# Kernel optimization log

Hardware: AMD Instinct MI355X
Metric: run time of the kernel (lower is better)

The kernel has to match this reference:

```python
import jax, jax.numpy as jnp
import numpy as np

N_OFFSETS = [(1, 0), (1, 1), (0, 1), (-1, 1), (-1, 0), (-1, -1), (0, -1), (1, -1)]
DILATION = 1


def setup_inputs() -> dict:
    key = jax.random.key(0)
    feats = jax.random.normal(key, (8, 128, 256, 256), dtype=jnp.float32)
    return {"feats": feats}


def reference(feats):
    # feats: [B, C, H, W]
    d = DILATION
    B, C, H, W = feats.shape
    # channel-wise L2 normalize (no eps, matching torch .norm division)
    normed = feats / jnp.linalg.norm(feats, axis=1, keepdims=True)
    # reflect pad last two spatial dims by d
    padded = jnp.pad(normed, ((0, 0), (0, 0), (d, d), (d, d)), mode="reflect")
    # 8 shifted multiply + channel-sum correlations (fixed small offset set)
    corrs = jnp.concatenate(
        [
            jnp.sum(
                normed
                * padded[:, :, d - dx * d // d if False else d - dx:H + d - dx, d - dy:W + d - dy],
                axis=1,
                keepdims=True,
            )
            for dx, dy in [(ox * d, oy * d) for ox, oy in N_OFFSETS]
        ],
        axis=1,
    )  # [B, 8, H, W]
    return corrs
```

## Files before the change

kernel.cpp:

```cpp
#include <hip/hip_runtime.h>


#define BB 8
#define CC 128
#define HH 256
#define WW 256
#define CSPLIT 2
#define CPW (CC / CSPLIT)

#define DD(k, j) acc[12 + (k)*4 + (j)]

__global__ __launch_bounds__(128) void featcorr_kernel(
    const float* __restrict__ feats, float* __restrict__ out) {
  const int lane = threadIdx.x;
  const int wy = threadIdx.y;
  const int h = (blockIdx.x % 8) * (HH / 8) + (blockIdx.x / 8);
  const int b = blockIdx.y;

  const int hm = (h == 0) ? 1 : h - 1;
  const int hp = (h == HH - 1) ? HH - 2 : h + 1;

  const size_t HW = (size_t)HH * WW;
  const int col0 = lane * 4;

  const float* pT = feats + ((size_t)b * CC + wy * CPW) * HW + (size_t)hm * WW + col0;
  const float* pM = feats + ((size_t)b * CC + wy * CPW) * HW + (size_t)h * WW + col0;
  const float* pB = feats + ((size_t)b * CC + wy * CPW) * HW + (size_t)hp * WW + col0;

  float acc[44];
#pragma unroll
  for (int a = 0; a < 44; ++a) acc[a] = 0.f;

  auto compute = [&](const float4 t, const float4 m, const float4 bt) {
    const float rT = __shfl_down(t.x, 1);
    const float rM = __shfl_down(m.x, 1);
    const float rB = __shfl_down(bt.x, 1);
    acc[0] += t.x * t.x;  acc[1] += t.y * t.y;  acc[2] += t.z * t.z;  acc[3] += t.w * t.w;
    acc[4] += m.x * m.x;  acc[5] += m.y * m.y;  acc[6] += m.z * m.z;  acc[7] += m.w * m.w;
    acc[8] += bt.x * bt.x; acc[9] += bt.y * bt.y; acc[10] += bt.z * bt.z; acc[11] += bt.w * bt.w;
    DD(0, 0) += m.x * t.x; DD(0, 1) += m.y * t.y; DD(0, 2) += m.z * t.z; DD(0, 3) += m.w * t.w;
    DD(4, 0) += m.x * bt.x; DD(4, 1) += m.y * bt.y; DD(4, 2) += m.z * bt.z; DD(4, 3) += m.w * bt.w;
    DD(1, 1) += m.y * t.x; DD(1, 2) += m.z * t.y; DD(1, 3) += m.w * t.z;
    DD(1, 0) += rM * t.w;
    DD(2, 1) += m.y * m.x; DD(2, 2) += m.z * m.y; DD(2, 3) += m.w * m.z;
    DD(2, 0) += rM * m.w;
    DD(3, 1) += m.y * bt.x; DD(3, 2) += m.z * bt.y; DD(3, 3) += m.w * bt.z;
    DD(3, 0) += rM * bt.w;
    DD(5, 0) += m.x * bt.y; DD(5, 1) += m.y * bt.z; DD(5, 2) += m.z * bt.w; DD(5, 3) += m.w * rB;
    DD(6, 0) += m.x * m.y; DD(6, 1) += m.y * m.z; DD(6, 2) += m.z * m.w; DD(6, 3) += m.w * rM;
    DD(7, 0) += m.x * t.y; DD(7, 1) += m.y * t.z; DD(7, 2) += m.z * t.w; DD(7, 3) += m.w * rT;
  };

  float4 tA = *(const float4*)pT, mA = *(const float4*)pM, bA = *(const float4*)pB;
  pT += HW; pM += HW; pB += HW;
  float4 tB = *(const float4*)pT, mB = *(const float4*)pM, bB = *(const float4*)pB;
  pT += HW; pM += HW; pB += HW;

#pragma unroll 2
  for (int c = 0; c < CPW - 2; ++c) {
    const float4 tC = *(const float4*)pT;
    const float4 mC = *(const float4*)pM;
    const float4 bC = *(const float4*)pB;
    pT += HW; pM += HW; pB += HW;
    compute(tA, mA, bA);
    tA = tB; mA = mB; bA = bB;
    tB = tC; mB = mC; bB = bC;
  }
  compute(tA, mA, bA);
  compute(tB, mB, bB);

  __shared__ float lds[44][64];
  if (wy == 1) {
#pragma unroll
    for (int a = 0; a < 44; ++a) lds[a][lane] = acc[a];
  }
  __syncthreads();

  if (wy == 0) {
#pragma unroll
    for (int a = 0; a < 44; ++a) acc[a] += lds[a][lane];

    const float g1 = __shfl_up(DD(1, 0), 1);
    const float g2 = __shfl_up(DD(2, 0), 1);
    const float g3 = __shfl_up(DD(3, 0), 1);
    DD(1, 0) = (lane == 0) ? DD(7, 0) : g1;
    DD(2, 0) = (lane == 0) ? DD(6, 0) : g2;
    DD(3, 0) = (lane == 0) ? DD(5, 0) : g3;
    if (lane == 63) {
      DD(5, 3) = DD(3, 3);
      DD(6, 3) = DD(2, 3);
      DD(7, 3) = DD(1, 3);
    }

    float it[4], im[4], ib[4];
#pragma unroll
    for (int j = 0; j < 4; ++j) {
      it[j] = rsqrtf(acc[j]);
      im[j] = rsqrtf(acc[4 + j]);
      ib[j] = rsqrtf(acc[8 + j]);
    }
    float IT[6], IM[6], IB[6];
    IT[1] = it[0]; IT[2] = it[1]; IT[3] = it[2]; IT[4] = it[3];
    IM[1] = im[0]; IM[2] = im[1]; IM[3] = im[2]; IM[4] = im[3];
    IB[1] = ib[0]; IB[2] = ib[1]; IB[3] = ib[2]; IB[4] = ib[3];
    const float tl = __shfl_up(it[3], 1), ml = __shfl_up(im[3], 1), bl = __shfl_up(ib[3], 1);
    const float tr = __shfl_down(it[0], 1), mr = __shfl_down(im[0], 1), br = __shfl_down(ib[0], 1);
    IT[0] = (lane == 0) ? it[1] : tl;
    IM[0] = (lane == 0) ? im[1] : ml;
    IB[0] = (lane == 0) ? ib[1] : bl;
    IT[5] = (lane == 63) ? it[2] : tr;
    IM[5] = (lane == 63) ? im[2] : mr;
    IB[5] = (lane == 63) ? ib[2] : br;

    float* obase = out + ((size_t)b * 8) * HW + (size_t)h * WW + col0;
#pragma unroll
    for (int k = 0; k < 8; ++k) {
      float v[4];
#pragma unroll
      for (int j = 0; j < 4; ++j) {
        float in;
        switch (k) {
          case 0: in = it[j];     break;
          case 1: in = IT[j];     break;
          case 2: in = IM[j];     break;
          case 3: in = IB[j];     break;
          case 4: in = ib[j];     break;
          case 5: in = IB[j + 2]; break;
          case 6: in = IM[j + 2]; break;
          default: in = IT[j + 2]; break;
        }
        v[j] = DD(k, j) * im[j] * in;
      }
      float4 o;
      o.x = v[0]; o.y = v[1]; o.z = v[2]; o.w = v[3];
      *(float4*)(obase + (size_t)k * HW) = o;
    }
  }
}

extern "C" void kernel_launch(void* const* d_in, const int* in_sizes, int n_in,
                              void* d_out, int out_size, void* d_ws, size_t ws_size,
                              hipStream_t stream) {
  const float* feats = (const float*)d_in[0];
  float* out = (float*)d_out;
  dim3 block(64, CSPLIT, 1);
  dim3 grid(HH, BB, 1);
  featcorr_kernel<<<grid, block, 0, stream>>>(feats, out);
}
```

Baseline: 365.8 us.

## Process four rows per block with LDS-staged shared halo rows

Each block now handles four output rows with eight wavefronts (four rows times two channel halves). Each wave loads one or two input rows per channel and stages them in double-buffered LDS so the six rows are shared, rather than every row reloading its three neighbours from global memory. The redundant DD(2,0) accumulation is dropped and recovered from DD(6,3) of the left lane. This cuts global read amplification from 3x to 1.5x, at the cost of two block barriers per channel pair and more LDS traffic.

Result: no change. 367.2 us (+0.4%).

```diff
diff --git a/kernel.cpp b/kernel.cpp
--- a/kernel.cpp
+++ b/kernel.cpp
@@ -5,33 +5,59 @@
 #define CC 128
 #define HH 256
 #define WW 256
-#define CSPLIT 2
-#define CPW (CC / CSPLIT)
+#define RR 4
+#define NV 6
+#define CPH (CC / 2)
 
 #define DD(k, j) acc[12 + (k)*4 + (j)]
 
-__global__ __launch_bounds__(128) void featcorr_kernel(
+union SmemU {
+  float stage[2][2][NV][WW];
+  float red[RR][44][64];
+};
+
+__global__ __launch_bounds__(512) void featcorr_kernel(
     const float* __restrict__ feats, float* __restrict__ out) {
+  __shared__ SmemU sm;
   const int lane = threadIdx.x;
   const int wy = threadIdx.y;
-  const int h = (blockIdx.x % 8) * (HH / 8) + (blockIdx.x / 8);
+  const int r = wy & 3;
+  const int cs = wy >> 2;
+  const int bx = blockIdx.x;
+  const int h0 = (((bx & 7) << 3) | (bx >> 3)) * RR;
   const int b = blockIdx.y;
-
-  const int hm = (h == 0) ? 1 : h - 1;
-  const int hp = (h == HH - 1) ? HH - 2 : h + 1;
+  const int h = h0 + r;
 
   const size_t HW = (size_t)HH * WW;
   const int col0 = lane * 4;
 
-  const float* pT = feats + ((size_t)b * CC + wy * CPW) * HW + (size_t)hm * WW + col0;
-  const float* pM = feats + ((size_t)b * CC + wy * CPW) * HW + (size_t)h * WW + col0;
-  const float* pB = feats + ((size_t)b * CC + wy * CPW) * HW + (size_t)hp * WW + col0;
+  int g1 = h0 - 1 + r;
+  if (g1 < 0) g1 = 1;
+  const bool two = (r < 2);
+  int g2 = h0 + 3 + r;
+  if (g2 >= HH) g2 = HH - 2;
+
+  const float* base = feats + ((size_t)b * CC + (size_t)cs * CPH) * HW + col0;
+  const float* p1 = base + (size_t)g1 * WW;
+  const float* p2 = base + (size_t)g2 * WW;
 
   float acc[44];
 #pragma unroll
   for (int a = 0; a < 44; ++a) acc[a] = 0.f;
 
-  auto compute = [&](const float4 t, const float4 m, const float4 bt) {
+  auto gload = [&](int c, float4& a1, float4& a2) {
+    a1 = *(const float4*)(p1 + (size_t)c * HW);
+    if (two) a2 = *(const float4*)(p2 + (size_t)c * HW);
+  };
+  auto stage = [&](int buf, const float4 a1, const float4 a2) {
+    *(float4*)&sm.stage[buf][cs][r][col0] = a1;
+    if (two) *(float4*)&sm.stage[buf][cs][4 + r][col0] = a2;
+  };
+
+  auto compute = [&](int buf) {
+    const float4 t = *(const float4*)&sm.stage[buf][cs][r][col0];
+    const float4 m = *(const float4*)&sm.stage[buf][cs][r + 1][col0];
+    const float4 bt = *(const float4*)&sm.stage[buf][cs][r + 2][col0];
     const float rT = __shfl_down(t.x, 1);
     const float rM = __shfl_down(m.x, 1);
     const float rB = __shfl_down(bt.x, 1);
@@ -43,7 +69,6 @@
     DD(1, 1) += m.y * t.x; DD(1, 2) += m.z * t.y; DD(1, 3) += m.w * t.z;
     DD(1, 0) += rM * t.w;
     DD(2, 1) += m.y * m.x; DD(2, 2) += m.z * m.y; DD(2, 3) += m.w * m.z;
-    DD(2, 0) += rM * m.w;
     DD(3, 1) += m.y * bt.x; DD(3, 2) += m.z * bt.y; DD(3, 3) += m.w * bt.z;
     DD(3, 0) += rM * bt.w;
     DD(5, 0) += m.x * bt.y; DD(5, 1) += m.y * bt.z; DD(5, 2) += m.z * bt.w; DD(5, 3) += m.w * rB;
@@ -51,41 +76,40 @@
     DD(7, 0) += m.x * t.y; DD(7, 1) += m.y * t.z; DD(7, 2) += m.z * t.w; DD(7, 3) += m.w * rT;
   };
 
-  float4 tA = *(const float4*)pT, mA = *(const float4*)pM, bA = *(const float4*)pB;
-  pT += HW; pM += HW; pB += HW;
-  float4 tB = *(const float4*)pT, mB = *(const float4*)pM, bB = *(const float4*)pB;
-  pT += HW; pM += HW; pB += HW;
+  float4 s0a, s0b = make_float4(0, 0, 0, 0);
+  float4 s1a, s1b = make_float4(0, 0, 0, 0);
+  gload(0, s0a, s0b);
+  gload(1, s1a, s1b);
+  stage(0, s0a, s0b);
+  __syncthreads();
 
-#pragma unroll 2
-  for (int c = 0; c < CPW - 2; ++c) {
-    const float4 tC = *(const float4*)pT;
-    const float4 mC = *(const float4*)pM;
-    const float4 bC = *(const float4*)pB;
-    pT += HW; pM += HW; pB += HW;
-    compute(tA, mA, bA);
-    tA = tB; mA = mB; bA = bB;
-    tB = tC; mB = mC; bB = bC;
+  for (int c = 0; c < CPH; c += 2) {
+    if (c + 2 < CPH) gload(c + 2, s0a, s0b);
+    stage(1, s1a, s1b);
+    compute(0);
+    __syncthreads();
+    if (c + 3 < CPH) gload(c + 3, s1a, s1b);
+    if (c + 2 < CPH) stage(0, s0a, s0b);
+    compute(1);
+    __syncthreads();
   }
-  compute(tA, mA, bA);
-  compute(tB, mB, bB);
 
-  __shared__ float lds[44][64];
-  if (wy == 1) {
+  if (cs == 1) {
 #pragma unroll
-    for (int a = 0; a < 44; ++a) lds[a][lane] = acc[a];
+    for (int a = 0; a < 44; ++a) sm.red[r][a][lane] = acc[a];
   }
   __syncthreads();
 
-  if (wy == 0) {
+  if (cs == 0) {
 #pragma unroll
-    for (int a = 0; a < 44; ++a) acc[a] += lds[a][lane];
+    for (int a = 0; a < 44; ++a) acc[a] += sm.red[r][a][lane];
 
-    const float g1 = __shfl_up(DD(1, 0), 1);
-    const float g2 = __shfl_up(DD(2, 0), 1);
-    const float g3 = __shfl_up(DD(3, 0), 1);
-    DD(1, 0) = (lane == 0) ? DD(7, 0) : g1;
-    DD(2, 0) = (lane == 0) ? DD(6, 0) : g2;
-    DD(3, 0) = (lane == 0) ? DD(5, 0) : g3;
+    const float g1v = __shfl_up(DD(1, 0), 1);
+    const float g2v = __shfl_up(DD(6, 3), 1);
+    const float g3v = __shfl_up(DD(3, 0), 1);
+    DD(1, 0) = (lane == 0) ? DD(7, 0) : g1v;
+    DD(2, 0) = (lane == 0) ? DD(6, 0) : g2v;
+    DD(3, 0) = (lane == 0) ? DD(5, 0) : g3v;
     if (lane == 63) {
       DD(5, 3) = DD(3, 3);
       DD(6, 3) = DD(2, 3);
@@ -143,7 +167,7 @@
                               hipStream_t stream) {
   const float* feats = (const float*)d_in[0];
   float* out = (float*)d_out;
-  dim3 block(64, CSPLIT, 1);
-  dim3 grid(HH, BB, 1);
+  dim3 block(64, 8, 1);
+  dim3 grid(HH / RR, BB, 1);
   featcorr_kernel<<<grid, block, 0, stream>>>(feats, out);
 }
```
